# Kernel tuning notes

Hardware: AMD Instinct MI355X
Metric: run time of the kernel (lower is better)

The kernel has to match this reference:

```python
import jax, jax.numpy as jnp
import numpy as np

V, D, H, L, T, B = 32000, 512, 8, 4, 2048, 2
HS = D // H


def setup_inputs() -> dict:
    key = jax.random.key(0)
    ks = jax.random.split(key, 10)
    s = 0.02  # init std, per _init_weights
    rn = lambda k, shape: jax.random.normal(k, shape, jnp.float32) * s
    return {
        "idx": jax.random.randint(ks[0], (B, T), 0, V),
        "tok_emb": rn(ks[1], (V, D)),
        "pos_emb": rn(ks[2], (T, D)),
        "ln1_g": jnp.ones((L, D)), "ln1_b": jnp.zeros((L, D)),
        "wq": rn(ks[3], (L, D, D)), "wk": rn(ks[4], (L, D, D)), "wv": rn(ks[5], (L, D, D)),
        "wo": rn(ks[6], (L, D, D)), "bo": jnp.zeros((L, D)),
        "ln2_g": jnp.ones((L, D)), "ln2_b": jnp.zeros((L, D)),
        "w1": rn(ks[7], (L, D, 4 * D)), "b1": jnp.zeros((L, 4 * D)),
        "w2": rn(ks[8], (L, 4 * D, D)), "b2": jnp.zeros((L, D)),
        "lnf_g": jnp.ones((D,)), "lnf_b": jnp.zeros((D,)),
        "head_w": rn(ks[9], (D, V)), "head_b": jnp.zeros((V,)),
    }


def _ln(x, g, b):
    mu = x.mean(-1, keepdims=True)
    var = ((x - mu) ** 2).mean(-1, keepdims=True)
    return (x - mu) * jax.lax.rsqrt(var + 1e-5) * g + b


def reference(idx, tok_emb, pos_emb, ln1_g, ln1_b, wq, wk, wv, wo, bo,
              ln2_g, ln2_b, w1, b1, w2, b2, lnf_g, lnf_b, head_w, head_b):
    Bb, Tt = idx.shape
    x = tok_emb[idx] + pos_emb[jnp.arange(Tt)]  # [B,T,D]
    mask = jnp.tril(jnp.ones((Tt, Tt), bool))
    scale = HS ** -0.5

    def block(x, p):
        g1, bb1, Wq, Wk, Wv, Wo, Bo, g2, bb2, W1, B1, W2, B2 = p
        h = _ln(x, g1, bb1)
        q = (h @ Wq).reshape(Bb, Tt, H, HS)
        k = (h @ Wk).reshape(Bb, Tt, H, HS)
        v = (h @ Wv).reshape(Bb, Tt, H, HS)
        wei = jnp.einsum('bthd,bshd->bhts', q, k) * scale  # [B,H,T,T]
        wei = jnp.where(mask, wei, -jnp.inf)
        wei = jax.nn.softmax(wei, axis=-1)
        att = jnp.einsum('bhts,bshd->bthd', wei, v).reshape(Bb, Tt, D)
        x = x + att @ Wo + Bo
        h2 = _ln(x, g2, bb2)
        x = x + jax.nn.relu(h2 @ W1 + B1) @ W2 + B2
        return x, None

    x, _ = jax.lax.scan(block, x, (ln1_g, ln1_b, wq, wk, wv, wo, bo,
                                   ln2_g, ln2_b, w1, b1, w2, b2))
    logits = _ln(x, lnf_g, lnf_b) @ head_w + head_b  # [B,T,V]
    return logits
```

## Files before the change

kernel.cpp:

```cpp
#include <hip/hip_runtime.h>
#include <hip/hip_bf16.h>
#include <cstddef>

typedef __bf16 bf16;
typedef __attribute__((ext_vector_type(8))) __bf16 bf16x8;
typedef __attribute__((ext_vector_type(4))) __bf16 bf16x4;
typedef __attribute__((ext_vector_type(4))) float f32x4;

constexpr int VOC = 32000;
constexpr int DIM = 512;
constexpr int NH  = 8;
constexpr int HSZ = 64;
constexpr int SEQ = 2048;
constexpr int NB  = 2;
constexpr int NL  = 4;
constexpr int NTOK = NB * SEQ;
constexpr int QS  = 3 * DIM;
constexpr int QKS = 2 * DIM;

__device__ __forceinline__ void gload16(const void* g, void* lds) {
  __builtin_amdgcn_global_load_lds(
      (const __attribute__((address_space(1))) unsigned int*)g,
      (__attribute__((address_space(3))) unsigned int*)lds, 16, 0, 0);
}

__global__ __launch_bounds__(256) void wt_emln(
    const int* __restrict__ idx, const float* __restrict__ tok,
    const float* __restrict__ pos, const float* __restrict__ g1,
    const float* __restrict__ b1v, float* __restrict__ x, bf16* __restrict__ h,
    const float* __restrict__ wq, const float* __restrict__ wk,
    const float* __restrict__ wv, const float* __restrict__ wo,
    const float* __restrict__ w1, const float* __restrict__ w2,
    const float* __restrict__ hw,
    bf16* __restrict__ wqkvT, bf16* __restrict__ woT,
    bf16* __restrict__ w1T, bf16* __restrict__ w2T, bf16* __restrict__ headT) {
  __shared__ float t[64][65];
  __shared__ float s1[4], s2[4];
  int bid = blockIdx.x;
  int tid = threadIdx.x;
  if (bid < NTOK) {
    int row = bid;
    int lane = tid & 63, w = tid >> 6;
    int tt = row & (SEQ - 1);
    int tk = idx[row];
    float a0 = tok[(size_t)tk * DIM + tid] + pos[(size_t)tt * DIM + tid];
    float a1 = tok[(size_t)tk * DIM + tid + 256] + pos[(size_t)tt * DIM + tid + 256];
    x[(size_t)row * DIM + tid] = a0;
    x[(size_t)row * DIM + tid + 256] = a1;
    float ps = a0 + a1, pq = a0 * a0 + a1 * a1;
#pragma unroll
    for (int m = 1; m < 64; m <<= 1) {
      ps += __shfl_xor(ps, m, 64);
      pq += __shfl_xor(pq, m, 64);
    }
    if (lane == 0) { s1[w] = ps; s2[w] = pq; }
    __syncthreads();
    float fs = s1[0] + s1[1] + s1[2] + s1[3];
    float fq = s2[0] + s2[1] + s2[2] + s2[3];
    float mu = fs * (1.0f / DIM);
    float var = fq * (1.0f / DIM) - mu * mu;
    float rs = rsqrtf(var + 1e-5f);
    h[(size_t)row * DIM + tid] = (bf16)((a0 - mu) * rs * g1[tid] + b1v[tid]);
    h[(size_t)row * DIM + tid + 256] =
        (bf16)((a1 - mu) * rs * g1[tid + 256] + b1v[tid + 256]);
    return;
  }
  int wb = bid - NTOK;
  const float* src; bf16* dst; int K, N, n0, k0;
  if (wb < 3072) {
    int l = wb / 768, tt = wb - l * 768;
    if (tt < 256) {
      int which = tt >> 6, u = tt & 63;
      K = DIM; N = DIM;
      n0 = (u & 7) * 64; k0 = (u >> 3) * 64;
      if (which == 0)      { src = wq + (size_t)l * DIM * DIM; dst = wqkvT + (size_t)l * QS * DIM; }
      else if (which == 1) { src = wk + (size_t)l * DIM * DIM; dst = wqkvT + (size_t)l * QS * DIM + DIM * DIM; }
      else if (which == 2) { src = wv + (size_t)l * DIM * DIM; dst = wqkvT + (size_t)l * QS * DIM + 2 * DIM * DIM; }
      else                 { src = wo + (size_t)l * DIM * DIM; dst = woT + (size_t)l * DIM * DIM; }
    } else if (tt < 512) {
      int u = tt - 256;
      K = DIM; N = 4 * DIM;
      n0 = (u & 31) * 64; k0 = (u >> 5) * 64;
      src = w1 + (size_t)l * DIM * 4 * DIM; dst = w1T + (size_t)l * 4 * DIM * DIM;
    } else {
      int u = tt - 512;
      K = 4 * DIM; N = DIM;
      n0 = (u & 7) * 64; k0 = (u >> 3) * 64;
      src = w2 + (size_t)l * 4 * DIM * DIM; dst = w2T + (size_t)l * 4 * DIM * DIM;
    }
  } else {
    int u = wb - 3072;
    K = DIM; N = VOC;
    n0 = (u >> 3) * 64; k0 = (u & 7) * 64;
    src = hw; dst = headT;
  }
  int tx = tid & 63, ty = tid >> 6;
#pragma unroll
  for (int r = 0; r < 16; ++r) {
    int row = ty + r * 4;
    t[row][tx] = src[(size_t)(k0 + row) * N + n0 + tx];
  }
  __syncthreads();
#pragma unroll
  for (int r = 0; r < 16; ++r) {
    int row = ty + r * 4;
    dst[(size_t)(n0 + row) * K + k0 + tx] = (bf16)t[tx][row];
  }
}

__global__ __launch_bounds__(256) void ln_kernel(
    const float* __restrict__ x, const float* __restrict__ g,
    const float* __restrict__ b, bf16* __restrict__ out) {
  int row = blockIdx.x * 4 + (threadIdx.x >> 6);
  int lane = threadIdx.x & 63;
  const float* xr = x + (size_t)row * DIM + lane * 8;
  float4 v0 = *(const float4*)xr;
  float4 v1 = *(const float4*)(xr + 4);
  float ps = v0.x + v0.y + v0.z + v0.w + v1.x + v1.y + v1.z + v1.w;
  float pq = v0.x * v0.x + v0.y * v0.y + v0.z * v0.z + v0.w * v0.w +
             v1.x * v1.x + v1.y * v1.y + v1.z * v1.z + v1.w * v1.w;
#pragma unroll
  for (int m = 1; m < 64; m <<= 1) {
    ps += __shfl_xor(ps, m, 64);
    pq += __shfl_xor(pq, m, 64);
  }
  float mu = ps * (1.0f / DIM);
  float var = pq * (1.0f / DIM) - mu * mu;
  float rs = rsqrtf(var + 1e-5f);
  const float* gp = g + lane * 8;
  const float* bp = b + lane * 8;
  float4 g0 = *(const float4*)gp, g1v = *(const float4*)(gp + 4);
  float4 b0 = *(const float4*)bp, b1v = *(const float4*)(bp + 4);
  bf16x8 o;
  o[0] = (bf16)((v0.x - mu) * rs * g0.x + b0.x);
  o[1] = (bf16)((v0.y - mu) * rs * g0.y + b0.y);
  o[2] = (bf16)((v0.z - mu) * rs * g0.z + b0.z);
  o[3] = (bf16)((v0.w - mu) * rs * g0.w + b0.w);
  o[4] = (bf16)((v1.x - mu) * rs * g1v.x + b1v.x);
  o[5] = (bf16)((v1.y - mu) * rs * g1v.y + b1v.y);
  o[6] = (bf16)((v1.z - mu) * rs * g1v.z + b1v.z);
  o[7] = (bf16)((v1.w - mu) * rs * g1v.w + b1v.w);
  *(bf16x8*)(out + (size_t)row * DIM + lane * 8) = o;
}

template <int BM, int BN, bool RELU, bool RES, bool OUTB, bool VSPLIT, bool DB>
__global__ __launch_bounds__((BN == 256) ? 512 : 256) void gemm_t(
    const bf16* __restrict__ A, const bf16* __restrict__ Wt,
    const float* __restrict__ bias, const float* __restrict__ res,
    float* __restrict__ outF, bf16* __restrict__ outB, bf16* __restrict__ vTout,
    int K, int N, int ostride) {
  constexpr int NW = (BN == 256) ? 8 : 4;
  constexpr int WN = (BN == 256) ? 4 : (BN == 128) ? 2 : 1;
  constexpr int WM = NW / WN;
  constexpr int MP = BM / WM / 16;
  constexpr int NP = BN / WN / 16;
  constexpr int AJ = (BM * 128) / (NW * 1024);
  constexpr int BJ = (BN * 128) / (NW * 1024);
  constexpr int VC = AJ + BJ;
  static_assert(!DB || VC == 6 || VC == 8, "DB vmcnt supports 6 or 8 loads");
  __shared__ bf16 As[(DB ? 2 : 1) * BM * 64];
  __shared__ bf16 Bs[(DB ? 2 : 1) * BN * 64];
  int tid = threadIdx.x;
  int wid = tid >> 6, ln = tid & 63;
  int lr = ln & 15, lg = ln >> 4;
  int nmt = gridDim.x;
  int bid = blockIdx.y * nmt + blockIdx.x;
  int cpx = (gridDim.x * gridDim.y) >> 3;
  int swz = (bid & 7) * cpx + (bid >> 3);
  int m0 = (swz % nmt) * BM;
  int n0 = (swz / nmt) * BN;
  int wr = wid / WN, wc = wid % WN;
  f32x4 acc[MP][NP] = {};

  const char* Ab = (const char*)A;
  const char* Bb = (const char*)Wt;

  auto STAGE = [&](int k0s, int buf) {
#pragma unroll
    for (int j = 0; j < AJ; ++j) {
      int Lb = j * (NW * 1024) + wid * 1024;
      int L = Lb + ln * 16;
      int row = L >> 7;
      int colb = (L & 127) ^ ((row & 7) << 4);
      gload16(Ab + (size_t)(m0 + row) * (K * 2) + (size_t)k0s * 2 + colb,
              (char*)As + buf * (BM * 128) + Lb);
    }
#pragma unroll
    for (int j = 0; j < BJ; ++j) {
      int Lb = j * (NW * 1024) + wid * 1024;
      int L = Lb + ln * 16;
      int row = L >> 7;
      int colb = (L & 127) ^ ((row & 7) << 4);
      gload16(Bb + (size_t)(n0 + row) * (K * 2) + (size_t)k0s * 2 + colb,
              (char*)Bs + buf * (BN * 128) + Lb);
    }
  };

  if (DB) STAGE(0, 0);
  int cur = 0;
  for (int k0 = 0; k0 < K; k0 += 64) {
    if (!DB) {
      __syncthreads();
      STAGE(k0, 0);
      __syncthreads();
    } else {
      if (k0 + 64 < K) {
        STAGE(k0 + 64, cur ^ 1);
        if constexpr (VC == 6)
          asm volatile("s_waitcnt vmcnt(6)" ::: "memory");
        else
          asm volatile("s_waitcnt vmcnt(8)" ::: "memory");
      } else {
        asm volatile("s_waitcnt vmcnt(0)" ::: "memory");
      }
      __builtin_amdgcn_s_barrier();
    }
#pragma unroll
    for (int kk = 0; kk < 2; ++kk) {
      bf16x8 am[MP], bn[NP];
#pragma unroll
      for (int m = 0; m < MP; ++m) {
        int row = wr * (BM / WM) + m * 16 + lr;
        int cb = (kk * 64 + lg * 16) ^ ((row & 7) << 4);
        am[m] = *(const bf16x8*)((const char*)As + cur * (BM * 128) + row * 128 + cb);
      }
#pragma unroll
      for (int n = 0; n < NP; ++n) {
        int row = wc * (BN / WN) + n * 16 + lr;
        int cb = (kk * 64 + lg * 16) ^ ((row & 7) << 4);
        bn[n] = *(const bf16x8*)((const char*)Bs + cur * (BN * 128) + row * 128 + cb);
      }
#pragma unroll
      for (int m = 0; m < MP; ++m)
#pragma unroll
        for (int n = 0; n < NP; ++n)
          acc[m][n] = __builtin_amdgcn_mfma_f32_16x16x32_bf16(
              am[m], bn[n], acc[m][n], 0, 0, 0);
    }
    if (DB) {
      __builtin_amdgcn_s_barrier();
      cur ^= 1;
    }
  }

  if (VSPLIT && n0 >= 2 * DIM) {
#pragma unroll
    for (int m = 0; m < MP; ++m) {
      int mrow = m0 + wr * (BM / WM) + m * 16 + lg * 4;
      int bb = mrow >> 11, tt = mrow & (SEQ - 1);
#pragma unroll
      for (int n = 0; n < NP; ++n) {
        int d = n0 + wc * (BN / WN) + n * 16 + lr - 2 * DIM;
        bf16x4 pk;
#pragma unroll
        for (int i = 0; i < 4; ++i) pk[i] = (bf16)acc[m][n][i];
        *(bf16x4*)(vTout + ((size_t)(bb * NH + (d >> 6)) * HSZ + (d & 63)) * SEQ + tt) = pk;
      }
    }
    return;
  }

  float qscale = (VSPLIT && n0 < DIM) ? 0.125f : 1.0f;
#pragma unroll
  for (int m = 0; m < MP; ++m) {
    int mrow = m0 + wr * (BM / WM) + m * 16 + lg * 4;
#pragma unroll
    for (int n = 0; n < NP; ++n) {
      int nc = n0 + wc * (BN / WN) + n * 16 + lr;
      float bval = bias ? bias[nc] : 0.0f;
#pragma unroll
      for (int i = 0; i < 4; ++i) {
        int mm = mrow + i;
        float val = acc[m][n][i] * qscale + bval;
        if (RELU) val = fmaxf(val, 0.0f);
        if (RES) val += res[(size_t)mm * ostride + nc];
        if (OUTB) outB[(size_t)mm * ostride + nc] = (bf16)val;
        else      outF[(size_t)mm * ostride + nc] = val;
      }
    }
  }
}

__global__ __launch_bounds__(256) void fattn_kernel(
    const bf16* __restrict__ qk, const bf16* __restrict__ vT,
    bf16* __restrict__ att) {
  __shared__ bf16 Ks[2][64 * 64];
  __shared__ bf16 Vs[2][64 * 64];
  __shared__ bf16 Pl[4][16][72];
  int tid = threadIdx.x;
  int wave = tid >> 6, lane = tid & 63;
  int lr = lane & 15, lg = lane >> 4;
  int h = blockIdx.y, b = blockIdx.z;
  int qt0 = ((b == 1) ? (gridDim.x - 1 - blockIdx.x) : blockIdx.x) * 64;
  const bf16* qb = qk + ((size_t)b * SEQ) * QKS + h * HSZ;
  const char* kb = (const char*)(qb + DIM);
  const char* vb = (const char*)(vT + (size_t)(b * NH + h) * HSZ * SEQ);

  bf16x8 aq[2];
  {
    const bf16* qr = qb + (size_t)(qt0 + wave * 16 + lr) * QKS + lg * 8;
    aq[0] = *(const bf16x8*)qr;
    aq[1] = *(const bf16x8*)(qr + 32);
  }

  f32x4 accO[4] = {};
  float l_r[4] = {0.f, 0.f, 0.f, 0.f};

  int ntile = qt0 / 64 + 1;
#define STAGE(ti, buf)                                                        \
  {                                                                           \
    _Pragma("unroll")                                                         \
    for (int j = 0; j < 2; ++j) {                                             \
      int Lb = j * 4096 + wave * 1024;                                        \
      int L = Lb + lane * 16;                                                 \
      int row = L >> 7;                                                       \
      int cb = (L & 127) ^ ((row & 7) << 4);                                  \
      gload16(kb + (size_t)((ti) * 64 + row) * (QKS * 2) + cb,                \
              (char*)Ks[buf] + Lb);                                           \
      gload16(vb + (size_t)row * (SEQ * 2) + (ti) * 128 + cb,                 \
              (char*)Vs[buf] + Lb);                                           \
    }                                                                         \
  }

  STAGE(0, 0);
  int cur = 0;
  for (int ti = 0; ti < ntile; ++ti) {
    if (ti + 1 < ntile) {
      STAGE(ti + 1, cur ^ 1);
      asm volatile("s_waitcnt vmcnt(4)" ::: "memory");
    } else {
      asm volatile("s_waitcnt vmcnt(0)" ::: "memory");
    }
    __builtin_amdgcn_s_barrier();
    int kv0 = ti * 64;
    bool diag = (ti == ntile - 1);

    f32x4 sc[4];
    __builtin_amdgcn_s_setprio(1);
#pragma unroll
    for (int s = 0; s < 4; ++s) {
      int row = s * 16 + lr;
      const char* base = (const char*)Ks[cur] + row * 128;
      bf16x8 b0 = *(const bf16x8*)(base + ((lg * 16) ^ ((row & 7) << 4)));
      bf16x8 b1 = *(const bf16x8*)(base + ((64 + lg * 16) ^ ((row & 7) << 4)));
      f32x4 z = {};
      z = __builtin_amdgcn_mfma_f32_16x16x32_bf16(aq[0], b0, z, 0, 0, 0);
      sc[s] = __builtin_amdgcn_mfma_f32_16x16x32_bf16(aq[1], b1, z, 0, 0, 0);
    }
    __builtin_amdgcn_s_setprio(0);

#pragma unroll
    for (int i = 0; i < 4; ++i) {
      if (diag) {
        int qrow = qt0 + wave * 16 + lg * 4 + i;
#pragma unroll
        for (int s = 0; s < 4; ++s) {
          int kvc = kv0 + s * 16 + lr;
          if (kvc > qrow) sc[s][i] = -1e30f;
        }
      }
      float rs = 0.f;
#pragma unroll
      for (int s = 0; s < 4; ++s) {
        float p = __expf(sc[s][i]);
        sc[s][i] = p;
        rs += p;
      }
      rs += __shfl_xor(rs, 1, 64);
      rs += __shfl_xor(rs, 2, 64);
      rs += __shfl_xor(rs, 4, 64);
      rs += __shfl_xor(rs, 8, 64);
      l_r[i] += rs;
    }

#pragma unroll
    for (int i = 0; i < 4; ++i)
#pragma unroll
      for (int s = 0; s < 4; ++s)
        Pl[wave][lg * 4 + i][s * 16 + lr] = (bf16)sc[s][i];
    bf16x8 pa0 = *(const bf16x8*)&Pl[wave][lr][lg * 8];
    bf16x8 pa1 = *(const bf16x8*)&Pl[wave][lr][32 + lg * 8];

    __builtin_amdgcn_s_setprio(1);
#pragma unroll
    for (int ds = 0; ds < 4; ++ds) {
      int row = ds * 16 + lr;
      const char* base = (const char*)Vs[cur] + row * 128;
      bf16x8 v0 = *(const bf16x8*)(base + ((lg * 16) ^ ((row & 7) << 4)));
      bf16x8 v1 = *(const bf16x8*)(base + ((64 + lg * 16) ^ ((row & 7) << 4)));
      accO[ds] = __builtin_amdgcn_mfma_f32_16x16x32_bf16(pa0, v0, accO[ds], 0, 0, 0);
      accO[ds] = __builtin_amdgcn_mfma_f32_16x16x32_bf16(pa1, v1, accO[ds], 0, 0, 0);
    }
    __builtin_amdgcn_s_setprio(0);
    __builtin_amdgcn_s_barrier();
    cur ^= 1;
  }
#undef STAGE

#pragma unroll
  for (int i = 0; i < 4; ++i) {
    float inv = 1.0f / l_r[i];
    size_t orow = ((size_t)b * SEQ + qt0 + wave * 16 + lg * 4 + i) * DIM + h * HSZ;
#pragma unroll
    for (int ds = 0; ds < 4; ++ds)
      att[orow + ds * 16 + lr] = (bf16)(accO[ds][i] * inv);
  }
}

extern "C" void kernel_launch(void* const* d_in, const int* in_sizes, int n_in,
                              void* d_out, int out_size, void* d_ws, size_t ws_size,
                              hipStream_t stream) {
  const int*   idx    = (const int*)d_in[0];
  const float* tok    = (const float*)d_in[1];
  const float* pos    = (const float*)d_in[2];
  const float* ln1_g  = (const float*)d_in[3];
  const float* ln1_b  = (const float*)d_in[4];
  const float* wq     = (const float*)d_in[5];
  const float* wk     = (const float*)d_in[6];
  const float* wv     = (const float*)d_in[7];
  const float* wo     = (const float*)d_in[8];
  const float* bo     = (const float*)d_in[9];
  const float* ln2_g  = (const float*)d_in[10];
  const float* ln2_b  = (const float*)d_in[11];
  const float* w1     = (const float*)d_in[12];
  const float* b1     = (const float*)d_in[13];
  const float* w2     = (const float*)d_in[14];
  const float* b2     = (const float*)d_in[15];
  const float* lnf_g  = (const float*)d_in[16];
  const float* lnf_b  = (const float*)d_in[17];
  const float* head_w = (const float*)d_in[18];
  const float* head_b = (const float*)d_in[19];

  char* W = (char*)d_ws;
  float* x     = (float*)(W);
  bf16*  h     = (bf16*)(W + 8388608);
  bf16*  qk    = (bf16*)(W + 12582912);
  bf16*  vTb   = (bf16*)(W + 20971520);
  bf16*  attb  = (bf16*)(W + 25165824);
  bf16*  ffn   = (bf16*)(W + 29360128);
  bf16*  wqkvT = (bf16*)(W + 46137344);
  bf16*  woT   = (bf16*)(W + 52428800);
  bf16*  w1T   = (bf16*)(W + 54525952);
  bf16*  w2T   = (bf16*)(W + 62914560);
  bf16*  headT = (bf16*)(W + 71303168);

  wt_emln<<<NTOK + 3072 + 4000, 256, 0, stream>>>(
      idx, tok, pos, ln1_g, ln1_b, x, h,
      wq, wk, wv, wo, w1, w2, head_w, wqkvT, woT, w1T, w2T, headT);

  dim3 gQKV(NTOK / 128, QS / 128);
  dim3 gD64(NTOK / 128, DIM / 64);
  dim3 gF1(NTOK / 128, 4 * DIM / 128);
  dim3 gV(NTOK / 128, VOC / 256);
  dim3 gA(SEQ / 64, NH, NB);

  for (int l = 0; l < NL; ++l) {
    if (l > 0)
      ln_kernel<<<NTOK / 4, 256, 0, stream>>>(x, ln1_g + l * DIM, ln1_b + l * DIM, h);
    gemm_t<128, 128, false, false, true, true, true><<<gQKV, 256, 0, stream>>>(
        h, wqkvT + (size_t)l * QS * DIM, nullptr, nullptr, nullptr, qk, vTb,
        DIM, QS, QKS);
    fattn_kernel<<<gA, 256, 0, stream>>>(qk, vTb, attb);
    gemm_t<128, 64, false, true, false, false, true><<<gD64, 256, 0, stream>>>(
        attb, woT + (size_t)l * DIM * DIM, bo + l * DIM, x, x, nullptr, nullptr,
        DIM, DIM, DIM);
    ln_kernel<<<NTOK / 4, 256, 0, stream>>>(x, ln2_g + l * DIM, ln2_b + l * DIM, h);
    gemm_t<128, 128, true, false, true, false, true><<<gF1, 256, 0, stream>>>(
        h, w1T + (size_t)l * 4 * DIM * DIM, b1 + (size_t)l * 4 * DIM, nullptr,
        nullptr, ffn, nullptr, DIM, 4 * DIM, 4 * DIM);
    gemm_t<128, 64, false, true, false, false, true><<<gD64, 256, 0, stream>>>(
        ffn, w2T + (size_t)l * 4 * DIM * DIM, b2 + l * DIM, x, x, nullptr,
        nullptr, 4 * DIM, DIM, DIM);
  }

  ln_kernel<<<NTOK / 4, 256, 0, stream>>>(x, lnf_g, lnf_b, h);
  gemm_t<128, 256, false, false, false, false, false><<<gV, 512, 0, stream>>>(
      h, headT, head_b, nullptr, (float*)d_out, nullptr, nullptr, DIM, VOC, VOC);
}
```

Measured before the change: 788.7 us.

## Add dedicated 256x256 double-buffered head GEMM kernel with staged prefetch

```diff
diff --git a/kernel.cpp b/kernel.cpp
--- a/kernel.cpp
+++ b/kernel.cpp
@@ -144,13 +144,13 @@
 }
 
 template <int BM, int BN, bool RELU, bool RES, bool OUTB, bool VSPLIT, bool DB>
-__global__ __launch_bounds__((BN == 256) ? 512 : 256) void gemm_t(
+__global__ __launch_bounds__(256) void gemm_t(
     const bf16* __restrict__ A, const bf16* __restrict__ Wt,
     const float* __restrict__ bias, const float* __restrict__ res,
     float* __restrict__ outF, bf16* __restrict__ outB, bf16* __restrict__ vTout,
     int K, int N, int ostride) {
-  constexpr int NW = (BN == 256) ? 8 : 4;
-  constexpr int WN = (BN == 256) ? 4 : (BN == 128) ? 2 : 1;
+  constexpr int NW = 4;
+  constexpr int WN = (BN == 128) ? 2 : 1;
   constexpr int WM = NW / WN;
   constexpr int MP = BM / WM / 16;
   constexpr int NP = BN / WN / 16;
@@ -277,6 +277,103 @@
         if (OUTB) outB[(size_t)mm * ostride + nc] = (bf16)val;
         else      outF[(size_t)mm * ostride + nc] = val;
       }
+    }
+  }
+}
+
+__global__ __launch_bounds__(512) void gemm_head(
+    const bf16* __restrict__ A, const bf16* __restrict__ Wt,
+    const float* __restrict__ bias, float* __restrict__ out, int K, int N) {
+  __shared__ bf16 As[2][256 * 64];
+  __shared__ bf16 Bs[2][256 * 64];
+  int tid = threadIdx.x;
+  int wid = tid >> 6, ln = tid & 63;
+  int lr = ln & 15, lg = ln >> 4;
+  int nmt = gridDim.x;
+  int bid = blockIdx.y * nmt + blockIdx.x;
+  int cpx = (gridDim.x * gridDim.y) >> 3;
+  int swz = (bid & 7) * cpx + (bid >> 3);
+  int m0 = (swz % nmt) * 256;
+  int n0 = (swz / nmt) * 256;
+  int wr = wid >> 2, wc = wid & 3;
+  f32x4 acc[8][4] = {};
+  const char* Ab = (const char*)A;
+  const char* Bb = (const char*)Wt;
+
+  auto STG = [&](int kt, int ht, int buf) {
+#pragma unroll
+    for (int c = 0; c < 2; ++c) {
+      int Lb = (ht & 1) * 16384 + c * 8192 + wid * 1024;
+      int L = Lb + ln * 16;
+      int row = L >> 7;
+      int colb = (L & 127) ^ ((row & 7) << 4);
+      const char* src = (ht < 2 ? Ab + (size_t)(m0 + row) * (K * 2)
+                                : Bb + (size_t)(n0 + row) * (K * 2)) +
+                        (size_t)(kt * 64) * 2 + colb;
+      gload16(src, (char*)(ht < 2 ? As[buf] : Bs[buf]) + Lb);
+    }
+  };
+
+  int nkt = K / 64;
+  STG(0, 0, 0); STG(0, 1, 0); STG(0, 2, 0); STG(0, 3, 0);
+  for (int t = 0; t < nkt; ++t) {
+    int buf = t & 1;
+    bf16x8 bn[4][2];
+#pragma unroll
+    for (int p = 0; p < 4; ++p) {
+      if (p == 0) {
+        if (t + 1 < nkt) {
+          STG(t + 1, 0, buf ^ 1);
+          asm volatile("s_waitcnt vmcnt(2)" ::: "memory");
+        } else {
+          asm volatile("s_waitcnt vmcnt(0)" ::: "memory");
+        }
+        __builtin_amdgcn_s_barrier();
+#pragma unroll
+        for (int n = 0; n < 4; ++n)
+#pragma unroll
+          for (int kk = 0; kk < 2; ++kk) {
+            int row = wc * 64 + n * 16 + lr;
+            int cb = (kk * 64 + lg * 16) ^ ((row & 7) << 4);
+            bn[n][kk] = *(const bf16x8*)((const char*)Bs[buf] + row * 128 + cb);
+          }
+      } else {
+        if (t + 1 < nkt) STG(t + 1, p, buf ^ 1);
+      }
+      bf16x8 am[2][2];
+#pragma unroll
+      for (int m = 0; m < 2; ++m)
+#pragma unroll
+        for (int kk = 0; kk < 2; ++kk) {
+          int row = wr * 128 + p * 32 + m * 16 + lr;
+          int cb = (kk * 64 + lg * 16) ^ ((row & 7) << 4);
+          am[m][kk] = *(const bf16x8*)((const char*)As[buf] + row * 128 + cb);
+        }
+      __builtin_amdgcn_s_setprio(1);
+#pragma unroll
+      for (int m = 0; m < 2; ++m)
+#pragma unroll
+        for (int n = 0; n < 4; ++n) {
+          acc[p * 2 + m][n] = __builtin_amdgcn_mfma_f32_16x16x32_bf16(
+              am[m][0], bn[n][0], acc[p * 2 + m][n], 0, 0, 0);
+          acc[p * 2 + m][n] = __builtin_amdgcn_mfma_f32_16x16x32_bf16(
+              am[m][1], bn[n][1], acc[p * 2 + m][n], 0, 0, 0);
+        }
+      __builtin_amdgcn_s_setprio(0);
+    }
+    __builtin_amdgcn_s_barrier();
+  }
+
+#pragma unroll
+  for (int m = 0; m < 8; ++m) {
+    int mrow = m0 + wr * 128 + m * 16 + lg * 4;
+#pragma unroll
+    for (int n = 0; n < 4; ++n) {
+      int nc = n0 + wc * 64 + n * 16 + lr;
+      float bval = bias[nc];
+#pragma unroll
+      for (int i = 0; i < 4; ++i)
+        out[(size_t)(mrow + i) * N + nc] = acc[m][n][i] + bval;
     }
   }
 }
@@ -451,7 +548,7 @@
   dim3 gQKV(NTOK / 128, QS / 128);
   dim3 gD64(NTOK / 128, DIM / 64);
   dim3 gF1(NTOK / 128, 4 * DIM / 128);
-  dim3 gV(NTOK / 128, VOC / 256);
+  dim3 gV(NTOK / 256, VOC / 256);
   dim3 gA(SEQ / 64, NH, NB);
 
   for (int l = 0; l < NL; ++l) {
@@ -474,6 +571,5 @@
   }
 
   ln_kernel<<<NTOK / 4, 256, 0, stream>>>(x, lnf_g, lnf_b, h);
-  gemm_t<128, 256, false, false, false, false, false><<<gV, 512, 0, stream>>>(
-      h, headT, head_b, nullptr, (float*)d_out, nullptr, nullptr, DIM, VOC, VOC);
-}
+  gemm_head<<<gV, 512, 0, stream>>>(h, headT, head_b, (float*)d_out, DIM, VOC);
+}
```

After: 817.3 us. 3.6% more time.
